# Optimization experiments

Measured on AMD Instinct MI355X. Metric: run time of the kernel, lower is better.

## Reference

```python
import jax, jax.numpy as jnp
import numpy as np

EPS = 1e-5
K = 7        # deformable/spatial kernel size
GRID = 4     # local pool grid size


def conv(x, w, pad=0):
    # x: NCHW, w: OIHW
    return jax.lax.conv_general_dilated(
        x, w, (1, 1), [(pad, pad), (pad, pad)],
        dimension_numbers=('NCHW', 'OIHW', 'NCHW'))


def bn(x, g, b, m, v):
    # eval-mode batchnorm with running stats
    scale = (g * jax.lax.rsqrt(v + EPS))[None, :, None, None]
    return (x - m[None, :, None, None]) * scale + b[None, :, None, None]


def grid_sample(feat, grid):
    # bilinear, padding_mode='zeros', align_corners=False
    # feat: [b,c,h,w], grid: [b,h,w,2] with (x,y) in [-1,1]
    b, c, h, w = feat.shape
    gx = (grid[..., 0] + 1.0) * (w * 0.5) - 0.5
    gy = (grid[..., 1] + 1.0) * (h * 0.5) - 0.5
    x0 = jnp.floor(gx)
    y0 = jnp.floor(gy)
    wx = gx - x0
    wy = gy - y0
    feat_flat = feat.reshape(b, c, h * w)

    def gather(yi, xi):
        valid = (xi >= 0) & (xi < w) & (yi >= 0) & (yi < h)
        xi_c = jnp.clip(xi, 0, w - 1).astype(jnp.int32)
        yi_c = jnp.clip(yi, 0, h - 1).astype(jnp.int32)
        idx = (yi_c * w + xi_c).reshape(b, 1, h * w)
        vals = jnp.take_along_axis(feat_flat, idx, axis=2).reshape(b, c, h, w)
        return vals * valid[:, None].astype(feat.dtype)

    out = (gather(y0, x0) * ((1 - wx) * (1 - wy))[:, None]
           + gather(y0, x0 + 1) * (wx * (1 - wy))[:, None]
           + gather(y0 + 1, x0) * ((1 - wx) * wy)[:, None]
           + gather(y0 + 1, x0 + 1) * (wx * wy)[:, None])
    return out


def cmife_forward(x, align_w, align_g, align_b, align_m, align_v,
                  mlp_w1, mlp_w2, loc_w1, loc_w2, fusion_w,
                  off_w1, off_g, off_bt, off_m, off_v, off_w2, off_b2,
                  attn_w):
    # ---- align: 1x1 conv + BN + SiLU ----
    x = conv(x, align_w)
    x = bn(x, align_g, align_b, align_m, align_v)
    x = x * jax.nn.sigmoid(x)  # SiLU
    b_, c_, h_, w_ = x.shape

    # ---- LocalGlobalChannelAttention ----
    def mlp(z):
        return conv(jax.nn.relu(conv(z, mlp_w1)), mlp_w2)

    g_avg = mlp(jnp.mean(x, (2, 3), keepdims=True))
    g_max = mlp(jnp.max(x, (2, 3), keepdims=True))
    global_attn = g_avg + g_max
    # adaptive avg pool to GRIDxGRID (h,w divisible by GRID)
    loc = x.reshape(b_, c_, GRID, h_ // GRID, GRID, w_ // GRID).mean((3, 5))
    local_attn = conv(jax.nn.relu(conv(loc, loc_w1)), loc_w2)
    local_attn = local_attn.mean((2, 3), keepdims=True)
    alpha = jax.nn.sigmoid(fusion_w)
    ca = jax.nn.sigmoid(alpha * global_attn + (1 - alpha) * local_attn)
    x = ca * x

    # ---- DeformableSpatialAttention ----
    avg_out = jnp.mean(x, 1, keepdims=True)
    max_out = jnp.max(x, 1, keepdims=True)
    sf = jnp.concatenate([avg_out, max_out], axis=1)  # [b,2,h,w]
    o = jax.nn.relu(bn(conv(sf, off_w1, pad=1), off_g, off_bt, off_m, off_v))
    o = conv(o, off_w2, pad=1) + off_b2[None, :, None, None]  # [b,2*K*K,h,w]
    off = o.reshape(b_, 2, K * K, h_, w_).mean(2)             # [b,2,h,w]
    off = jnp.tanh(off) * 0.5
    off = jnp.transpose(off, (0, 2, 3, 1))                    # [b,h,w,2]
    gy, gx = jnp.meshgrid(jnp.linspace(-1.0, 1.0, h_),
                          jnp.linspace(-1.0, 1.0, w_), indexing='ij')
    base = jnp.stack([gx, gy], axis=-1)[None]                 # [1,h,w,2]
    dgrid = jnp.clip(base + off, -1.0, 1.0)
    sampled = grid_sample(sf, dgrid)                          # [b,2,h,w]
    sa = jax.nn.sigmoid(conv(sampled, attn_w, pad=K // 2))    # [b,1,h,w]
    return sa * x


def setup_inputs() -> dict:
    key = jax.random.key(0)
    ks = jax.random.split(key, 24)
    B, CIN, COUT, H, W, MID = 8, 256, 256, 160, 160, 16
    f = jnp.float32
    inp = {
        'x': jax.random.normal(ks[0], (B, CIN, H, W), f),
        'align_w': jax.random.normal(ks[1], (COUT, CIN, 1, 1), f) * 0.05,
        'align_g': jax.random.uniform(ks[2], (COUT,), f, 0.5, 1.5),
        'align_b': jax.random.normal(ks[3], (COUT,), f) * 0.1,
        'align_m': jax.random.normal(ks[4], (COUT,), f) * 0.1,
        'align_v': jax.random.uniform(ks[5], (COUT,), f, 0.5, 1.5),
        'mlp_w1': jax.random.normal(ks[6], (MID, COUT, 1, 1), f) * 0.1,
        'mlp_w2': jax.random.normal(ks[7], (COUT, MID, 1, 1), f) * 0.1,
        'loc_w1': jax.random.normal(ks[8], (MID, COUT, 1, 1), f) * 0.1,
        'loc_w2': jax.random.normal(ks[9], (COUT, MID, 1, 1), f) * 0.1,
        'fusion_w': jnp.float32(0.5),
        'off_w1': jax.random.normal(ks[10], (16, 2, 3, 3), f) * 0.1,
        'off_g': jax.random.uniform(ks[11], (16,), f, 0.5, 1.5),
        'off_bt': jax.random.normal(ks[12], (16,), f) * 0.1,
        'off_m': jax.random.normal(ks[13], (16,), f) * 0.1,
        'off_v': jax.random.uniform(ks[14], (16,), f, 0.5, 1.5),
        'off_w2': jax.random.normal(ks[15], (2 * K * K, 16, 3, 3), f) * 0.01,
        'off_b2': jax.random.normal(ks[16], (2 * K * K,), f) * 0.01,
        'attn_w': jax.random.normal(ks[17], (1, 2, K, K), f) * 0.1,
    }
    return inp


def reference(x, align_w, align_g, align_b, align_m, align_v,
              mlp_w1, mlp_w2, loc_w1, loc_w2, fusion_w,
              off_w1, off_g, off_bt, off_m, off_v, off_w2, off_b2,
              attn_w):
    return cmife_forward(x, align_w, align_g, align_b, align_m, align_v,
                         mlp_w1, mlp_w2, loc_w1, loc_w2, fusion_w,
                         off_w1, off_g, off_bt, off_m, off_v, off_w2, off_b2,
                         attn_w)
```

## Files before the change

kernel.cpp:

```cpp
#include <hip/hip_runtime.h>
#include <hip/hip_bf16.h>

#define HH 160
#define WW 160
#define HW 25600
#define NC 256
#define NB 8

typedef short short8 __attribute__((ext_vector_type(8)));
typedef float f32x4 __attribute__((ext_vector_type(4)));

__device__ __forceinline__ unsigned short f2bf(float f) {
    unsigned u = __float_as_uint(f);
    u += 0x7fffu + ((u >> 16) & 1u);
    return (unsigned short)(u >> 16);
}
__device__ __forceinline__ float bf2f(unsigned short h) {
    return __uint_as_float(((unsigned)h) << 16);
}

__global__ void k0_fold(const float* __restrict__ aw, const float* __restrict__ ag,
                        const float* __restrict__ ab, const float* __restrict__ am,
                        const float* __restrict__ av,
                        unsigned short* __restrict__ wph, unsigned short* __restrict__ wpl,
                        float* __restrict__ biasp) {
    int co = blockIdx.x, t = threadIdx.x;
    float sc = ag[co] * rsqrtf(av[co] + 1e-5f);
    float w = aw[co * 256 + t] * sc;
    unsigned short h = f2bf(w);
    wph[co * 256 + t] = h;
    wpl[co * 256 + t] = f2bf(w - bf2f(h));
    if (t == 0) biasp[co] = ab[co] - am[co] * sc;
}

__global__ void k0b_fold2(const float* __restrict__ ow2, const float* __restrict__ ob2,
                          float* __restrict__ weff, float* __restrict__ beff) {
    int t = threadIdx.x;
    if (t < 288) {
        int g = t / 144, r = t - g * 144;
        float s = 0.f;
        for (int q = 0; q < 49; q++) s += ow2[(size_t)(g * 49 + q) * 144 + r];
        weff[t] = s * (1.f / 49.f);
    }
    if (t < 2) {
        float s = 0.f;
        for (int q = 0; q < 49; q++) s += ob2[t * 49 + q];
        beff[t] = s * (1.f / 49.f);
    }
}

__global__ __launch_bounds__(256) void k1_gemm(
    const float* __restrict__ X, const unsigned short* __restrict__ Wph,
    const unsigned short* __restrict__ Wpl,
    const float* __restrict__ biasp, float* __restrict__ xal) {
    __shared__ unsigned short Ah[256 * 40];
    __shared__ unsigned short Al[256 * 40];
    __shared__ unsigned short Bh[64 * 40];
    __shared__ unsigned short Bl[64 * 40];

    int t = threadIdx.x;
    int n0 = blockIdx.x * 64;
    int b  = blockIdx.y;
    const float* Xb = X + (size_t)b * NC * HW;

    int lane = t & 63, wv = t >> 6;
    int lcol = lane & 15, lq = lane >> 4;

    f32x4 acc[4][4];
#pragma unroll
    for (int i = 0; i < 4; i++)
#pragma unroll
        for (int j = 0; j < 4; j++) { f32x4 z = {0.f, 0.f, 0.f, 0.f}; acc[i][j] = z; }

    int bn2 = t & 31;
    int bkq = t >> 5;

    for (int kk = 0; kk < 8; kk++) {
        int k0 = kk * 32;
#pragma unroll
        for (int i = 0; i < 8; i++) {
            int q = t + i * 256;
            int co = q >> 3, kq = q & 7;
            uint2 vh = *(const uint2*)(Wph + (size_t)co * 256 + k0 + kq * 4);
            uint2 vl = *(const uint2*)(Wpl + (size_t)co * 256 + k0 + kq * 4);
            *(uint2*)(&Ah[co * 40 + kq * 4]) = vh;
            *(uint2*)(&Al[co * 40 + kq * 4]) = vl;
        }
        {
            const float* src = Xb + (size_t)(k0 + bkq * 4) * HW + n0 + bn2 * 2;
            unsigned h0[2], h1[2], l0[2], l1[2];
#pragma unroll
            for (int j = 0; j < 2; j++) {
                float2 v0 = *(const float2*)(src + (size_t)(2 * j) * HW);
                float2 v1 = *(const float2*)(src + (size_t)(2 * j + 1) * HW);
                unsigned short a = f2bf(v0.x), bq = f2bf(v1.x);
                unsigned short c = f2bf(v0.y), d = f2bf(v1.y);
                h0[j] = (unsigned)a | ((unsigned)bq << 16);
                h1[j] = (unsigned)c | ((unsigned)d << 16);
                unsigned short la = f2bf(v0.x - bf2f(a)), lb = f2bf(v1.x - bf2f(bq));
                unsigned short lc = f2bf(v0.y - bf2f(c)), ld = f2bf(v1.y - bf2f(d));
                l0[j] = (unsigned)la | ((unsigned)lb << 16);
                l1[j] = (unsigned)lc | ((unsigned)ld << 16);
            }
            *(uint2*)(&Bh[(bn2 * 2) * 40 + bkq * 4])     = make_uint2(h0[0], h0[1]);
            *(uint2*)(&Bh[(bn2 * 2 + 1) * 40 + bkq * 4]) = make_uint2(h1[0], h1[1]);
            *(uint2*)(&Bl[(bn2 * 2) * 40 + bkq * 4])     = make_uint2(l0[0], l0[1]);
            *(uint2*)(&Bl[(bn2 * 2 + 1) * 40 + bkq * 4]) = make_uint2(l1[0], l1[1]);
        }
        __syncthreads();
        short8 afh[4], afl[4], bfh[4], bfl[4];
#pragma unroll
        for (int mt = 0; mt < 4; mt++) {
            afh[mt] = *(const short8*)(&Ah[(wv * 64 + mt * 16 + lcol) * 40 + lq * 8]);
            afl[mt] = *(const short8*)(&Al[(wv * 64 + mt * 16 + lcol) * 40 + lq * 8]);
        }
#pragma unroll
        for (int nt = 0; nt < 4; nt++) {
            bfh[nt] = *(const short8*)(&Bh[(nt * 16 + lcol) * 40 + lq * 8]);
            bfl[nt] = *(const short8*)(&Bl[(nt * 16 + lcol) * 40 + lq * 8]);
        }
#pragma unroll
        for (int mt = 0; mt < 4; mt++)
#pragma unroll
            for (int nt = 0; nt < 4; nt++) {
                acc[mt][nt] = __builtin_amdgcn_mfma_f32_16x16x32_bf16(
                    afh[mt], bfh[nt], acc[mt][nt], 0, 0, 0);
                acc[mt][nt] = __builtin_amdgcn_mfma_f32_16x16x32_bf16(
                    afh[mt], bfl[nt], acc[mt][nt], 0, 0, 0);
                acc[mt][nt] = __builtin_amdgcn_mfma_f32_16x16x32_bf16(
                    afl[mt], bfh[nt], acc[mt][nt], 0, 0, 0);
            }
        __syncthreads();
    }
#pragma unroll
    for (int mt = 0; mt < 4; mt++) {
#pragma unroll
        for (int r = 0; r < 4; r++) {
            int co = wv * 64 + mt * 16 + lq * 4 + r;
            float bias = biasp[co];
            size_t rowbase = ((size_t)b * NC + co) * HW + n0;
#pragma unroll
            for (int nt = 0; nt < 4; nt++) {
                int n = nt * 16 + lcol;
                float y = acc[mt][nt][r] + bias;
                float z = y / (1.f + __expf(-y));
                xal[rowbase + n] = z;
            }
        }
    }
}

__global__ void ka_stats(const float* __restrict__ xal,
                         float* __restrict__ cellsum, float* __restrict__ cellmax) {
    __shared__ float redS[256], redM[256];
    int bc = blockIdx.x;
    int t = threadIdx.x;
    int cell = t >> 4, s = t & 15;
    int ch = cell >> 2, cw = cell & 3;
    const float* base = xal + (size_t)bc * HW;
    float sm = 0.f, mx = -3.4e38f;
    for (int k = 0; k < 100; k++) {
        int idx = s + 16 * k;
        int r = idx / 40, col = idx - r * 40;
        float v = base[(ch * 40 + r) * 160 + cw * 40 + col];
        sm += v;
        mx = fmaxf(mx, v);
    }
    redS[t] = sm;
    redM[t] = mx;
    __syncthreads();
    if (s == 0) {
        float cs = 0.f, cm = -3.4e38f;
#pragma unroll
        for (int i = 0; i < 16; i++) {
            cs += redS[t + i];
            cm = fmaxf(cm, redM[t + i]);
        }
        cellsum[bc * 16 + cell] = cs;
        cellmax[bc * 16 + cell] = cm;
    }
}

__global__ void kb_attn(const float* __restrict__ cellsum, const float* __restrict__ cellmax,
                        const float* __restrict__ mw1, const float* __restrict__ mw2,
                        const float* __restrict__ lw1, const float* __restrict__ lw2,
                        const float* __restrict__ fw, float* __restrict__ ca) {
    __shared__ float avgS[256], maxS[256], locS[256 * 16], hid[32], hlS[256];
    int b = blockIdx.x, t = threadIdx.x;
    float s = 0.f, m = -3.4e38f;
#pragma unroll
    for (int cell = 0; cell < 16; cell++) {
        float cs = cellsum[(b * 256 + t) * 16 + cell];
        float cm = cellmax[(b * 256 + t) * 16 + cell];
        s += cs;
        m = fmaxf(m, cm);
        locS[t * 16 + cell] = cs * (1.f / 1600.f);
    }
    avgS[t] = s * (1.f / 25600.f);
    maxS[t] = m;
    __syncthreads();
    if (t < 32) {
        int j = t & 15;
        const float* w1 = mw1 + j * 256;
        const float* src = (t < 16) ? avgS : maxS;
        float h = 0.f;
        for (int c = 0; c < 256; c++) h += w1[c] * src[c];
        hid[t] = fmaxf(h, 0.f);
    }
    {
        int cell = t >> 4, j = t & 15;
        const float* w1 = lw1 + j * 256;
        float h = 0.f;
        for (int c = 0; c < 256; c++) h += w1[c] * locS[c * 16 + cell];
        hlS[t] = fmaxf(h, 0.f);
    }
    __syncthreads();
    float ga = 0.f, gm = 0.f;
#pragma unroll
    for (int j = 0; j < 16; j++) {
        float w2 = mw2[t * 16 + j];
        ga += w2 * hid[j];
        gm += w2 * hid[16 + j];
    }
    float la = 0.f;
#pragma unroll
    for (int cell = 0; cell < 16; cell++)
#pragma unroll
        for (int j = 0; j < 16; j++)
            la += lw2[t * 16 + j] * hlS[cell * 16 + j];
    float alpha = 1.f / (1.f + expf(-fw[0]));
    float pre = alpha * (ga + gm) + (1.f - alpha) * (la * (1.f / 16.f));
    ca[b * 256 + t] = 1.f / (1.f + expf(-pre));
}

__global__ void k3_sf(const float* __restrict__ xal,
                      const float* __restrict__ ca, float* __restrict__ sf) {
    __shared__ float cas[256];
    int b = blockIdx.y, t = threadIdx.x;
    cas[t] = ca[b * 256 + t];
    __syncthreads();
    int p = blockIdx.x * 256 + t;
    const float* base = xal + (size_t)b * NC * HW + p;
    float s0 = 0.f, m0 = -3.4e38f;
    for (int c = 0; c < 256; c++) {
        float a0 = cas[c] * base[(size_t)c * HW];
        s0 += a0;
        m0 = fmaxf(m0, a0);
    }
    sf[(size_t)b * 2 * HW + p]      = s0 * (1.f / 256.f);
    sf[(size_t)b * 2 * HW + HW + p] = m0;
}

__global__ void k4_conv1(const float* __restrict__ sf, const float* __restrict__ ow1,
                         const float* __restrict__ og, const float* __restrict__ obt,
                         const float* __restrict__ om, const float* __restrict__ ov,
                         float* __restrict__ o1) {
    __shared__ float wS[288], scS[16], shS[16];
    int b = blockIdx.y, t = threadIdx.x;
    for (int i = t; i < 288; i += 256) wS[i] = ow1[i];
    if (t < 16) {
        float sc = og[t] * rsqrtf(ov[t] + 1e-5f);
        scS[t] = sc;
        shS[t] = obt[t] - om[t] * sc;
    }
    __syncthreads();
    int p = blockIdx.x * 256 + t;
    int h = p / 160, w = p - h * 160;
    const float* a0 = sf + (size_t)b * 2 * HW;
    const float* a1 = a0 + HW;
    float in0[9], in1[9];
#pragma unroll
    for (int kh = 0; kh < 3; kh++)
#pragma unroll
        for (int kw = 0; kw < 3; kw++) {
            int hh = h + kh - 1, ww = w + kw - 1;
            bool ok = (hh >= 0) & (hh < 160) & (ww >= 0) & (ww < 160);
            int q = hh * 160 + ww;
            in0[kh * 3 + kw] = ok ? a0[q] : 0.f;
            in1[kh * 3 + kw] = ok ? a1[q] : 0.f;
        }
    float* outb = o1 + (size_t)b * 16 * HW + p;
#pragma unroll
    for (int j = 0; j < 16; j++) {
        float acc = 0.f;
#pragma unroll
        for (int k = 0; k < 9; k++)
            acc += wS[j * 18 + k] * in0[k] + wS[j * 18 + 9 + k] * in1[k];
        outb[(size_t)j * HW] = fmaxf(acc * scS[j] + shS[j], 0.f);
    }
}

__global__ void k5_sample(const float* __restrict__ o1, const float* __restrict__ weff,
                          const float* __restrict__ beff, const float* __restrict__ sf,
                          float* __restrict__ sampled) {
    __shared__ float tileS[16 * 18 * 18];
    __shared__ float wS[288];
    __shared__ float bS[2];
    int b = blockIdx.y, t = threadIdx.x;
    int ty0 = (blockIdx.x / 10) * 16, tx0 = (blockIdx.x % 10) * 16;
    const float* ob = o1 + (size_t)b * 16 * HW;
    for (int i = t; i < 288; i += 256) wS[i] = weff[i];
    if (t < 2) bS[t] = beff[t];
    for (int i = t; i < 16 * 18 * 18; i += 256) {
        int ci = i / 324, rem = i - ci * 324;
        int r = rem / 18, c = rem - r * 18;
        int gr = ty0 + r - 1, gc = tx0 + c - 1;
        bool ok = (gr >= 0) & (gr < 160) & (gc >= 0) & (gc < 160);
        tileS[i] = ok ? ob[(size_t)ci * HW + gr * 160 + gc] : 0.f;
    }
    __syncthreads();
    int ty = t >> 4, tx = t & 15;
    int h = ty0 + ty, w = tx0 + tx;
    int p = h * 160 + w;
    float s0 = bS[0], s1 = bS[1];
#pragma unroll
    for (int ci = 0; ci < 16; ci++) {
        const float* tb = &tileS[ci * 324 + ty * 18 + tx];
        const float* w0 = &wS[ci * 9];
        const float* w1 = &wS[144 + ci * 9];
#pragma unroll
        for (int kh = 0; kh < 3; kh++)
#pragma unroll
            for (int kw = 0; kw < 3; kw++) {
                float v = tb[kh * 18 + kw];
                s0 += w0[kh * 3 + kw] * v;
                s1 += w1[kh * 3 + kw] * v;
            }
    }
    float ox = tanhf(s0) * 0.5f;
    float oy = tanhf(s1) * 0.5f;
    float bx = w * (2.f / 159.f) - 1.f, by = h * (2.f / 159.f) - 1.f;
    float gxn = fminf(fmaxf(bx + ox, -1.f), 1.f);
    float gyn = fminf(fmaxf(by + oy, -1.f), 1.f);
    float gx = (gxn + 1.f) * 80.f - 0.5f;
    float gy = (gyn + 1.f) * 80.f - 0.5f;
    float x0f = floorf(gx), y0f = floorf(gy);
    float wx = gx - x0f, wy = gy - y0f;
    int ix0 = (int)x0f, iy0 = (int)y0f;
    const float* f0 = sf + (size_t)b * 2 * HW;
    const float* f1 = f0 + HW;
    float r0 = 0.f, r1 = 0.f;
#pragma unroll
    for (int dy = 0; dy < 2; dy++)
#pragma unroll
        for (int dx = 0; dx < 2; dx++) {
            int xi = ix0 + dx, yi = iy0 + dy;
            float wgt = (dx ? wx : 1.f - wx) * (dy ? wy : 1.f - wy);
            if ((xi >= 0) & (xi < 160) & (yi >= 0) & (yi < 160)) {
                int q = yi * 160 + xi;
                r0 += wgt * f0[q];
                r1 += wgt * f1[q];
            }
        }
    float* sb = sampled + (size_t)b * 2 * HW + p;
    sb[0] = r0;
    sb[HW] = r1;
}

__global__ void k5b_sa(const float* __restrict__ sampled, const float* __restrict__ attn_w,
                       float* __restrict__ sa) {
    __shared__ float wS[98];
    int b = blockIdx.y, t = threadIdx.x;
    if (t < 98) wS[t] = attn_w[t];
    __syncthreads();
    int p = blockIdx.x * 256 + t;
    int h = p / 160, w = p - h * 160;
    const float* s0 = sampled + (size_t)b * 2 * HW;
    const float* s1 = s0 + HW;
    float acc = 0.f;
#pragma unroll
    for (int kh = 0; kh < 7; kh++) {
        int hh = h + kh - 3;
        if (hh < 0 || hh >= 160) continue;
#pragma unroll
        for (int kw = 0; kw < 7; kw++) {
            int ww = w + kw - 3;
            if (ww < 0 || ww >= 160) continue;
            int q = hh * 160 + ww;
            acc += wS[kh * 7 + kw] * s0[q] + wS[49 + kh * 7 + kw] * s1[q];
        }
    }
    sa[(size_t)b * HW + p] = 1.f / (1.f + expf(-acc));
}

__global__ void k6_out(float* __restrict__ out, const float* __restrict__ ca,
                       const float* __restrict__ sa) {
    unsigned e = blockIdx.x * 256 + threadIdx.x;
    unsigned b = e / (256u * HW);
    unsigned rem = e - b * (256u * HW);
    unsigned c = rem / HW;
    unsigned p = rem - c * HW;
    float v = out[e];
    out[e] = ca[b * 256 + c] * sa[(size_t)b * HW + p] * v;
}

extern "C" void kernel_launch(void* const* d_in, const int* in_sizes, int n_in,
                              void* d_out, int out_size, void* d_ws, size_t ws_size,
                              hipStream_t stream) {
    const float* x       = (const float*)d_in[0];
    const float* align_w = (const float*)d_in[1];
    const float* align_g = (const float*)d_in[2];
    const float* align_b = (const float*)d_in[3];
    const float* align_m = (const float*)d_in[4];
    const float* align_v = (const float*)d_in[5];
    const float* mlp_w1  = (const float*)d_in[6];
    const float* mlp_w2  = (const float*)d_in[7];
    const float* loc_w1  = (const float*)d_in[8];
    const float* loc_w2  = (const float*)d_in[9];
    const float* fusion  = (const float*)d_in[10];
    const float* off_w1  = (const float*)d_in[11];
    const float* off_g   = (const float*)d_in[12];
    const float* off_bt  = (const float*)d_in[13];
    const float* off_m   = (const float*)d_in[14];
    const float* off_v   = (const float*)d_in[15];
    const float* off_w2  = (const float*)d_in[16];
    const float* off_b2  = (const float*)d_in[17];
    const float* attn_w  = (const float*)d_in[18];
    float* out = (float*)d_out;

    char* wsb = (char*)d_ws;
    size_t off = 0;
    auto alloc = [&](size_t bytes) -> void* {
        off = (off + 255) & ~(size_t)255;
        void* p = wsb + off;
        off += bytes;
        return p;
    };
    float* xal = out;
    unsigned short* wph = (unsigned short*)alloc(65536 * 2);
    unsigned short* wpl = (unsigned short*)alloc(65536 * 2);
    float* biasp   = (float*)alloc(256 * 4);
    float* cellsum = (float*)alloc(32768 * 4);
    float* cellmax = (float*)alloc(32768 * 4);
    float* ca      = (float*)alloc(2048 * 4);
    float* sf      = (float*)alloc((size_t)NB * 2 * HW * 4);
    float* o1      = (float*)alloc((size_t)NB * 16 * HW * 4);
    float* sampled = (float*)alloc((size_t)NB * 2 * HW * 4);
    float* sa      = (float*)alloc((size_t)NB * HW * 4);
    float* weff    = (float*)alloc(288 * 4);
    float* beff    = (float*)alloc(2 * 4);
    (void)ws_size; (void)in_sizes; (void)n_in; (void)out_size;

    k0_fold<<<dim3(256), 256, 0, stream>>>(align_w, align_g, align_b, align_m, align_v,
                                           wph, wpl, biasp);
    k0b_fold2<<<dim3(1), 320, 0, stream>>>(off_w2, off_b2, weff, beff);
    k1_gemm<<<dim3(400, 8), 256, 0, stream>>>(x, wph, wpl, biasp, xal);
    ka_stats<<<dim3(2048), 256, 0, stream>>>(xal, cellsum, cellmax);
    kb_attn<<<dim3(8), 256, 0, stream>>>(cellsum, cellmax, mlp_w1, mlp_w2,
                                         loc_w1, loc_w2, fusion, ca);
    k3_sf<<<dim3(100, 8), 256, 0, stream>>>(xal, ca, sf);
    k4_conv1<<<dim3(100, 8), 256, 0, stream>>>(sf, off_w1, off_g, off_bt, off_m, off_v, o1);
    k5_sample<<<dim3(100, 8), 256, 0, stream>>>(o1, weff, beff, sf, sampled);
    k5b_sa<<<dim3(100, 8), 256, 0, stream>>>(sampled, attn_w, sa);
    k6_out<<<dim3(204800), 256, 0, stream>>>(out, ca, sa);
}
```

Measured before the change: 756.1 us.

## Widen GEMM N-tile, load pre-packed weights via direct-to-LDS, vectorize output scale

The align GEMM tile grows from 64 to 128 pixels per block, halving the number of blocks and doubling reuse of the 256-channel weight tile in LDS. Weights are pre-packed by the fold kernel into a padded per-k-slice layout so they can be copied with global_load_lds straight into shared memory, skipping the register round-trip. The final scaling kernel processes four elements per thread with vector loads and stores. The larger accumulator array (128 floats per lane) raises register pressure, and occupancy may drop despite the launch-bounds hint.

```diff
diff --git a/kernel.cpp b/kernel.cpp
--- a/kernel.cpp
+++ b/kernel.cpp
@@ -22,14 +22,15 @@
 __global__ void k0_fold(const float* __restrict__ aw, const float* __restrict__ ag,
                         const float* __restrict__ ab, const float* __restrict__ am,
                         const float* __restrict__ av,
-                        unsigned short* __restrict__ wph, unsigned short* __restrict__ wpl,
+                        unsigned short* __restrict__ wpkh, unsigned short* __restrict__ wpkl,
                         float* __restrict__ biasp) {
     int co = blockIdx.x, t = threadIdx.x;
     float sc = ag[co] * rsqrtf(av[co] + 1e-5f);
     float w = aw[co * 256 + t] * sc;
     unsigned short h = f2bf(w);
-    wph[co * 256 + t] = h;
-    wpl[co * 256 + t] = f2bf(w - bf2f(h));
+    int kk = t >> 5, kq = t & 31;
+    wpkh[kk * 10240 + co * 40 + kq] = h;
+    wpkl[kk * 10240 + co * 40 + kq] = f2bf(w - bf2f(h));
     if (t == 0) biasp[co] = ab[co] - am[co] * sc;
 }
 
@@ -49,45 +50,51 @@
     }
 }
 
-__global__ __launch_bounds__(256) void k1_gemm(
+__global__ __launch_bounds__(256, 2) void k1_gemm(
     const float* __restrict__ X, const unsigned short* __restrict__ Wph,
     const unsigned short* __restrict__ Wpl,
     const float* __restrict__ biasp, float* __restrict__ xal) {
-    __shared__ unsigned short Ah[256 * 40];
-    __shared__ unsigned short Al[256 * 40];
-    __shared__ unsigned short Bh[64 * 40];
-    __shared__ unsigned short Bl[64 * 40];
+    __shared__ __align__(16) unsigned short Ah[10240];
+    __shared__ __align__(16) unsigned short Al[10240];
+    __shared__ __align__(16) unsigned short Bh[5120];
+    __shared__ __align__(16) unsigned short Bl[5120];
 
     int t = threadIdx.x;
-    int n0 = blockIdx.x * 64;
+    int n0 = blockIdx.x * 128;
     int b  = blockIdx.y;
     const float* Xb = X + (size_t)b * NC * HW;
 
     int lane = t & 63, wv = t >> 6;
     int lcol = lane & 15, lq = lane >> 4;
 
-    f32x4 acc[4][4];
+    f32x4 acc[4][8];
 #pragma unroll
     for (int i = 0; i < 4; i++)
 #pragma unroll
-        for (int j = 0; j < 4; j++) { f32x4 z = {0.f, 0.f, 0.f, 0.f}; acc[i][j] = z; }
-
-    int bn2 = t & 31;
-    int bkq = t >> 5;
+        for (int j = 0; j < 8; j++) { f32x4 z = {0.f, 0.f, 0.f, 0.f}; acc[i][j] = z; }
+
+    int bn2 = t & 63;
+    int bkq = t >> 6;
 
     for (int kk = 0; kk < 8; kk++) {
-        int k0 = kk * 32;
-#pragma unroll
-        for (int i = 0; i < 8; i++) {
-            int q = t + i * 256;
-            int co = q >> 3, kq = q & 7;
-            uint2 vh = *(const uint2*)(Wph + (size_t)co * 256 + k0 + kq * 4);
-            uint2 vl = *(const uint2*)(Wpl + (size_t)co * 256 + k0 + kq * 4);
-            *(uint2*)(&Ah[co * 40 + kq * 4]) = vh;
-            *(uint2*)(&Al[co * 40 + kq * 4]) = vl;
-        }
-        {
-            const float* src = Xb + (size_t)(k0 + bkq * 4) * HW + n0 + bn2 * 2;
+        const char* gah = (const char*)(Wph + kk * 10240);
+        const char* gal = (const char*)(Wpl + kk * 10240);
+#pragma unroll
+        for (int i = 0; i < 5; i++) {
+            int off = wv * 1024 + i * 4096;
+            __builtin_amdgcn_global_load_lds(
+                (const __attribute__((address_space(1))) unsigned int*)(gah + off + lane * 16),
+                (__attribute__((address_space(3))) unsigned int*)((char*)Ah + off),
+                16, 0, 0);
+            __builtin_amdgcn_global_load_lds(
+                (const __attribute__((address_space(1))) unsigned int*)(gal + off + lane * 16),
+                (__attribute__((address_space(3))) unsigned int*)((char*)Al + off),
+                16, 0, 0);
+        }
+#pragma unroll
+        for (int j2 = 0; j2 < 2; j2++) {
+            int kq = bkq + 4 * j2;
+            const float* src = Xb + (size_t)(kk * 32 + kq * 4) * HW + n0 + bn2 * 2;
             unsigned h0[2], h1[2], l0[2], l1[2];
 #pragma unroll
             for (int j = 0; j < 2; j++) {
@@ -102,34 +109,33 @@
                 l0[j] = (unsigned)la | ((unsigned)lb << 16);
                 l1[j] = (unsigned)lc | ((unsigned)ld << 16);
             }
-            *(uint2*)(&Bh[(bn2 * 2) * 40 + bkq * 4])     = make_uint2(h0[0], h0[1]);
-            *(uint2*)(&Bh[(bn2 * 2 + 1) * 40 + bkq * 4]) = make_uint2(h1[0], h1[1]);
-            *(uint2*)(&Bl[(bn2 * 2) * 40 + bkq * 4])     = make_uint2(l0[0], l0[1]);
-            *(uint2*)(&Bl[(bn2 * 2 + 1) * 40 + bkq * 4]) = make_uint2(l1[0], l1[1]);
+            *(uint2*)(&Bh[(bn2 * 2) * 40 + kq * 4])     = make_uint2(h0[0], h0[1]);
+            *(uint2*)(&Bh[(bn2 * 2 + 1) * 40 + kq * 4]) = make_uint2(h1[0], h1[1]);
+            *(uint2*)(&Bl[(bn2 * 2) * 40 + kq * 4])     = make_uint2(l0[0], l0[1]);
+            *(uint2*)(&Bl[(bn2 * 2 + 1) * 40 + kq * 4]) = make_uint2(l1[0], l1[1]);
         }
         __syncthreads();
-        short8 afh[4], afl[4], bfh[4], bfl[4];
+
+        short8 afh[4], afl[4];
 #pragma unroll
         for (int mt = 0; mt < 4; mt++) {
             afh[mt] = *(const short8*)(&Ah[(wv * 64 + mt * 16 + lcol) * 40 + lq * 8]);
             afl[mt] = *(const short8*)(&Al[(wv * 64 + mt * 16 + lcol) * 40 + lq * 8]);
         }
-#pragma unroll
-        for (int nt = 0; nt < 4; nt++) {
-            bfh[nt] = *(const short8*)(&Bh[(nt * 16 + lcol) * 40 + lq * 8]);
-            bfl[nt] = *(const short8*)(&Bl[(nt * 16 + lcol) * 40 + lq * 8]);
-        }
-#pragma unroll
-        for (int mt = 0; mt < 4; mt++)
-#pragma unroll
-            for (int nt = 0; nt < 4; nt++) {
+#pragma unroll 2
+        for (int nt = 0; nt < 8; nt++) {
+            short8 bh = *(const short8*)(&Bh[(nt * 16 + lcol) * 40 + lq * 8]);
+            short8 bl = *(const short8*)(&Bl[(nt * 16 + lcol) * 40 + lq * 8]);
+#pragma unroll
+            for (int mt = 0; mt < 4; mt++) {
                 acc[mt][nt] = __builtin_amdgcn_mfma_f32_16x16x32_bf16(
-                    afh[mt], bfh[nt], acc[mt][nt], 0, 0, 0);
+                    afh[mt], bh, acc[mt][nt], 0, 0, 0);
                 acc[mt][nt] = __builtin_amdgcn_mfma_f32_16x16x32_bf16(
-                    afh[mt], bfl[nt], acc[mt][nt], 0, 0, 0);
+                    afh[mt], bl, acc[mt][nt], 0, 0, 0);
                 acc[mt][nt] = __builtin_amdgcn_mfma_f32_16x16x32_bf16(
-                    afl[mt], bfh[nt], acc[mt][nt], 0, 0, 0);
+                    afl[mt], bh, acc[mt][nt], 0, 0, 0);
             }
+        }
         __syncthreads();
     }
 #pragma unroll
@@ -140,7 +146,7 @@
             float bias = biasp[co];
             size_t rowbase = ((size_t)b * NC + co) * HW + n0;
 #pragma unroll
-            for (int nt = 0; nt < 4; nt++) {
+            for (int nt = 0; nt < 8; nt++) {
                 int n = nt * 16 + lcol;
                 float y = acc[mt][nt][r] + bias;
                 float z = y / (1.f + __expf(-y));
@@ -385,13 +391,18 @@
 
 __global__ void k6_out(float* __restrict__ out, const float* __restrict__ ca,
                        const float* __restrict__ sa) {
-    unsigned e = blockIdx.x * 256 + threadIdx.x;
+    unsigned e4 = blockIdx.x * 256 + threadIdx.x;
+    unsigned e = e4 * 4;
     unsigned b = e / (256u * HW);
     unsigned rem = e - b * (256u * HW);
     unsigned c = rem / HW;
     unsigned p = rem - c * HW;
-    float v = out[e];
-    out[e] = ca[b * 256 + c] * sa[(size_t)b * HW + p] * v;
+    f32x4 v = *(f32x4*)(out + e);
+    f32x4 s = *(const f32x4*)(sa + (size_t)b * HW + p);
+    float cav = ca[b * 256 + c];
+#pragma unroll
+    for (int i = 0; i < 4; i++) v[i] = cav * s[i] * v[i];
+    *(f32x4*)(out + e) = v;
 }
 
 extern "C" void kernel_launch(void* const* d_in, const int* in_sizes, int n_in,
@@ -427,8 +438,8 @@
         return p;
     };
     float* xal = out;
-    unsigned short* wph = (unsigned short*)alloc(65536 * 2);
-    unsigned short* wpl = (unsigned short*)alloc(65536 * 2);
+    unsigned short* wph = (unsigned short*)alloc(81920 * 2);
+    unsigned short* wpl = (unsigned short*)alloc(81920 * 2);
     float* biasp   = (float*)alloc(256 * 4);
     float* cellsum = (float*)alloc(32768 * 4);
     float* cellmax = (float*)alloc(32768 * 4);
@@ -444,7 +455,7 @@
     k0_fold<<<dim3(256), 256, 0, stream>>>(align_w, align_g, align_b, align_m, align_v,
                                            wph, wpl, biasp);
     k0b_fold2<<<dim3(1), 320, 0, stream>>>(off_w2, off_b2, weff, beff);
-    k1_gemm<<<dim3(400, 8), 256, 0, stream>>>(x, wph, wpl, biasp, xal);
+    k1_gemm<<<dim3(200, 8), 256, 0, stream>>>(x, wph, wpl, biasp, xal);
     ka_stats<<<dim3(2048), 256, 0, stream>>>(xal, cellsum, cellmax);
     kb_attn<<<dim3(8), 256, 0, stream>>>(cellsum, cellmax, mlp_w1, mlp_w2,
                                          loc_w1, loc_w2, fusion, ca);
@@ -452,5 +463,5 @@
     k4_conv1<<<dim3(100, 8), 256, 0, stream>>>(sf, off_w1, off_g, off_bt, off_m, off_v, o1);
     k5_sample<<<dim3(100, 8), 256, 0, stream>>>(o1, weff, beff, sf, sampled);
     k5b_sa<<<dim3(100, 8), 256, 0, stream>>>(sampled, attn_w, sa);
-    k6_out<<<dim3(204800), 256, 0, stream>>>(out, ca, sa);
-}
+    k6_out<<<dim3(51200), 256, 0, stream>>>(out, ca, sa);
+}
```

Measured after the change: 1.331 ms. 76.0% more time.
